# Optimization experiments

Measured on AMD Instinct MI355X. Metric: run time of the kernel, lower is better.

## Reference

```python
import jax, jax.numpy as jnp
import numpy as np

EPS = 1e-3  # sscp_conv_group_norm_eps


def setup_inputs() -> dict:
    key = jax.random.key(0)
    k1, k2, k3 = jax.random.split(key, 3)
    audio_encodings = jax.random.normal(k1, (4, 1, 4096, 128), dtype=jnp.float32)
    # Conv2d(in=1, out=128, kernel=(3,3), stride=(2,2), bias=False), OIHW layout
    conv_w = jax.random.normal(k2, (128, 1, 3, 3), dtype=jnp.float32) * 0.1
    # AudioCumulativeGroupNorm per-channel scale (init ones; randomize slightly)
    norm_scale = jnp.ones((128,), dtype=jnp.float32) + 0.01 * jax.random.normal(k3, (128,), dtype=jnp.float32)
    return {"audio_encodings": audio_encodings, "conv_w": conv_w, "norm_scale": norm_scale}


def reference(audio_encodings, conv_w, norm_scale):
    # manual_padding = (0, 1, 1, 1) in torch F.pad order (W_left, W_right, H_top, H_bottom)
    x = jnp.pad(audio_encodings, ((0, 0), (0, 0), (1, 1), (0, 1)))
    # Conv2d stride (2,2), no padding, no bias
    y = jax.lax.conv_general_dilated(
        x, conv_w, window_strides=(2, 2), padding='VALID',
        dimension_numbers=('NCHW', 'OIHW', 'NCHW'))  # [B, C, T, F]
    # permute to [B, T, F, C] and normalize cumulatively over T (mask=None)
    h = jnp.transpose(y, (0, 2, 3, 1)).astype(jnp.float32)
    B, T, F, C = h.shape
    # cumulative count of elements per group at each t: (t+1) * F * C
    cnt = (jnp.arange(1, T + 1, dtype=jnp.float32) * (F * C)).reshape(1, T, 1, 1)
    cum_sum = jnp.cumsum(jnp.sum(h, axis=(2, 3), keepdims=True), axis=1)  # [B,T,1,1]
    cum_mean = cum_sum / cnt
    sq = jnp.sum((h - cum_mean) ** 2, axis=(2, 3), keepdims=True)
    cum_var = jnp.cumsum(sq, axis=1) / cnt
    normed = (h - cum_mean) * jax.lax.rsqrt(cum_var + EPS) * norm_scale  # scale per channel (last dim)
    out = jnp.transpose(normed, (0, 3, 1, 2))  # back to [B, C, T, F]
    return jax.nn.relu(out)
```

## Files before the change

### kernel.cpp

```cpp
#include <hip/hip_runtime.h>

#define X_H 4096
#define X_W 128
#define BATCH 4
#define CH 128
#define TT_OUT 2048
#define FF 64
#define EPS_GN 1e-3f

typedef float f4 __attribute__((ext_vector_type(4)));

#define S1_OFF 0
#define SS_OFF (BATCH*TT_OUT)

__global__ __launch_bounds__(256) void stats_kernel(const float* __restrict__ x,
                                                    const float* __restrict__ w,
                                                    float* __restrict__ ws) {
    __shared__ float wlds[CH*9];
    __shared__ float Ml[81];
    __shared__ float Wl[9];
    int tid = threadIdx.x;
#pragma unroll
    for (int i = tid; i < CH*9; i += 256) wlds[i] = w[i];
    __syncthreads();
    if (tid < 81) {
        int j = tid / 9, k = tid % 9;
        float acc = 0.f;
#pragma unroll 8
        for (int c = 0; c < CH; ++c) acc = fmaf(wlds[c*9 + j], wlds[c*9 + k], acc);
        Ml[tid] = acc;
    } else if (tid < 90) {
        int k = tid - 81;
        float acc = 0.f;
#pragma unroll 8
        for (int c = 0; c < CH; ++c) acc += wlds[c*9 + k];
        Wl[k] = acc;
    }
    __syncthreads();

    int fq = tid & 15;
    int tr = tid >> 4;
    int gt = blockIdx.x * 16 + tr;
    int t = gt & (TT_OUT - 1);
    int b = gt >> 11;
    const float* xb = x + (size_t)b * (X_H * X_W);

    float xr[3][9];
    int r0 = 2*t - 1;
#pragma unroll
    for (int kh = 0; kh < 3; ++kh) {
        int r = r0 + kh;
        if (r >= 0 && r < X_H) {
            const float* rp = xb + (size_t)r * X_W + 8*fq;
            f4 v0 = *(const f4*)rp;
            f4 v1 = *(const f4*)(rp + 4);
            xr[kh][0]=v0.x; xr[kh][1]=v0.y; xr[kh][2]=v0.z; xr[kh][3]=v0.w;
            xr[kh][4]=v1.x; xr[kh][5]=v1.y; xr[kh][6]=v1.z; xr[kh][7]=v1.w;
            xr[kh][8] = (fq == 15) ? 0.f : rp[8];
        } else {
#pragma unroll
            for (int k = 0; k < 9; ++k) xr[kh][k] = 0.f;
        }
    }

    float s1 = 0.f, ss = 0.f;
#pragma unroll
    for (int jf = 0; jf < 4; ++jf) {
        float tv[9];
#pragma unroll
        for (int kh = 0; kh < 3; ++kh)
#pragma unroll
            for (int kw = 0; kw < 3; ++kw)
                tv[kh*3+kw] = xr[kh][2*jf + kw];
#pragma unroll
        for (int k = 0; k < 9; ++k) s1 = fmaf(Wl[k], tv[k], s1);
#pragma unroll
        for (int j = 0; j < 9; ++j) {
            float tj = 0.f;
#pragma unroll
            for (int k = 0; k < 9; ++k) tj = fmaf(Ml[j*9+k], tv[k], tj);
            ss = fmaf(tv[j], tj, ss);
        }
    }
#pragma unroll
    for (int off = 1; off < 16; off <<= 1) {
        s1 += __shfl_xor(s1, off);
        ss += __shfl_xor(ss, off);
    }
    if (fq == 0) {
        ws[S1_OFF + gt] = s1;
        ws[SS_OFF + gt] = ss;
    }
}

#define T_TILE 16
#define CG 32
__global__ __launch_bounds__(256) void out_kernel(const float* __restrict__ x,
        const float* __restrict__ w, const float* __restrict__ scale,
        const float* __restrict__ ws, float* __restrict__ out) {
    __shared__ float wl[CG][9];
    __shared__ float sl[CG];
    __shared__ float redA[4], redB[4], redC[4];
    int tid = threadIdx.x;
    int lane = tid & 63;
    int wv = tid >> 6;
    int b = blockIdx.z;
    int c0 = blockIdx.y * CG;
    int t0 = blockIdx.x * T_TILE;

    for (int i = tid; i < CG*9; i += 256) wl[i/9][i%9] = w[c0*9 + i];
    if (tid < CG) sl[tid] = scale[c0 + tid];

    const float* S1 = ws + S1_OFF + b*TT_OUT;
    const float* SS = ws + SS_OFF + b*TT_OUT;
    const f4* S1v = (const f4*)S1;
    const f4* SSv = (const f4*)SS;
    f4 a0 = S1v[tid*2], a1 = S1v[tid*2+1];
    f4 e0 = SSv[tid*2], e1 = SSv[tid*2+1];
    float s1l[8] = {a0.x,a0.y,a0.z,a0.w,a1.x,a1.y,a1.z,a1.w};
    float ssl[8] = {e0.x,e0.y,e0.z,e0.w,e1.x,e1.y,e1.z,e1.w};
    int tau0 = tid * 8;
    float s1m[8];
    float tot = 0.f;
#pragma unroll
    for (int i = 0; i < 8; ++i) {
        s1m[i] = (tau0 + i < t0) ? s1l[i] : 0.f;
        tot += s1m[i];
    }
    float incl = tot;
#pragma unroll
    for (int off = 1; off < 64; off <<= 1) {
        float n = __shfl_up(incl, off);
        if (lane >= off) incl += n;
    }
    if (lane == 63) redA[wv] = incl;
    __syncthreads();
    float woff = 0.f;
    for (int w2 = 0; w2 < wv; ++w2) woff += redA[w2];
    float prefix = woff + incl - tot;

    float run = prefix;
    float sqp = 0.f;
#pragma unroll
    for (int i = 0; i < 8; ++i) {
        if (tau0 + i < t0) {
            run += s1l[i];
            float cnt = (float)(tau0 + i + 1) * 8192.f;
            float mu = run / cnt;
            sqp += ssl[i] - 2.f*mu*s1l[i] + 8192.f*mu*mu;
        }
    }
    float r1 = tot, r2 = sqp;
#pragma unroll
    for (int off = 32; off > 0; off >>= 1) {
        r1 += __shfl_xor(r1, off);
        r2 += __shfl_xor(r2, off);
    }
    if (lane == 0) { redB[wv] = r1; redC[wv] = r2; }
    __syncthreads();
    float base1 = redB[0] + redB[1] + redB[2] + redB[3];
    float base_sq = redC[0] + redC[1] + redC[2] + redC[3];

    int tr = tid >> 4;
    float run16 = base1, sq16 = base_sq;
    float mu_t = 0.f, istd_t = 0.f;
#pragma unroll
    for (int i = 0; i < T_TILE; ++i) {
        int t = t0 + i;
        float s1t = S1[t];
        float sst = SS[t];
        run16 += s1t;
        float cnt = (float)(t + 1) * 8192.f;
        float mu = run16 / cnt;
        sq16 += sst - 2.f*mu*s1t + 8192.f*mu*mu;
        if (i == tr) { mu_t = mu; istd_t = rsqrtf(sq16 / cnt + EPS_GN); }
    }

    int fq = tid & 15;
    int t = t0 + tr;
    const float* xb = x + (size_t)b * (X_H * X_W);

    float xr[3][9];
    int r0 = 2*t - 1;
#pragma unroll
    for (int kh = 0; kh < 3; ++kh) {
        int r = r0 + kh;
        if (r >= 0 && r < X_H) {
            const float* rp = xb + (size_t)r * X_W + 8*fq;
            f4 v0 = *(const f4*)rp;
            f4 v1 = *(const f4*)(rp + 4);
            xr[kh][0]=v0.x; xr[kh][1]=v0.y; xr[kh][2]=v0.z; xr[kh][3]=v0.w;
            xr[kh][4]=v1.x; xr[kh][5]=v1.y; xr[kh][6]=v1.z; xr[kh][7]=v1.w;
            xr[kh][8] = (fq == 15) ? 0.f : rp[8];
        } else {
#pragma unroll
            for (int k = 0; k < 9; ++k) xr[kh][k] = 0.f;
        }
    }

    float* ob = out + (((size_t)(b*CH + c0) * TT_OUT + t) * FF + 4*fq);
#pragma unroll
    for (int c = 0; c < CG; ++c) {
        float a  = istd_t * sl[c];
        float nb = -mu_t * a;
        f4 v;
#pragma unroll
        for (int jf = 0; jf < 4; ++jf) {
            float h = 0.f;
#pragma unroll
            for (int kh = 0; kh < 3; ++kh)
#pragma unroll
                for (int kw = 0; kw < 3; ++kw)
                    h = fmaf(wl[c][kh*3+kw], xr[kh][2*jf + kw], h);
            v[jf] = fmaxf(fmaf(h, a, nb), 0.f);
        }
        *(f4*)(ob + (size_t)c * (TT_OUT * FF)) = v;
    }
}

extern "C" void kernel_launch(void* const* d_in, const int* in_sizes, int n_in,
                              void* d_out, int out_size, void* d_ws, size_t ws_size,
                              hipStream_t stream) {
    const float* x     = (const float*)d_in[0];
    const float* w     = (const float*)d_in[1];
    const float* scale = (const float*)d_in[2];
    float* out = (float*)d_out;
    float* ws  = (float*)d_ws;

    stats_kernel<<<(BATCH*TT_OUT)/16, 256, 0, stream>>>(x, w, ws);
    out_kernel<<<dim3(TT_OUT/T_TILE, CH/CG, BATCH), 256, 0, stream>>>(x, w, scale, ws, out);
}
```

Baseline: 59.35 us.

## Fuse stats and output kernels into one cooperative kernel with grid sync

Merges the statistics pass and the normalize/output pass into a single cooperative launch of 512 blocks, separated by a grid-wide barrier, so one kernel launch and its gap are removed. Each block now handles all 128 channels for its 16 time steps instead of splitting channels across 4 blocks, which cuts redundant input loads and prefix-scan work but leaves far fewer blocks for the write-heavy output phase. The grid barrier and the fixed 512-block grid also require all blocks to be co-resident.

```diff
diff --git a/kernel.cpp b/kernel.cpp
--- a/kernel.cpp
+++ b/kernel.cpp
@@ -1,4 +1,7 @@
 #include <hip/hip_runtime.h>
+#include <hip/hip_cooperative_groups.h>
+
+namespace cg = cooperative_groups;
 
 #define X_H 4096
 #define X_W 128
@@ -7,22 +10,32 @@
 #define TT_OUT 2048
 #define FF 64
 #define EPS_GN 1e-3f
+#define T_TILE 16
 
 typedef float f4 __attribute__((ext_vector_type(4)));
 
 #define S1_OFF 0
 #define SS_OFF (BATCH*TT_OUT)
 
-__global__ __launch_bounds__(256) void stats_kernel(const float* __restrict__ x,
-                                                    const float* __restrict__ w,
-                                                    float* __restrict__ ws) {
+__global__ __launch_bounds__(256) void fused_kernel(const float* __restrict__ x,
+        const float* __restrict__ w, const float* __restrict__ scale,
+        float* __restrict__ ws, float* __restrict__ out) {
     __shared__ float wlds[CH*9];
+    __shared__ float sl[CH];
     __shared__ float Ml[81];
     __shared__ float Wl[9];
+    __shared__ float redA[4], redB[4], redC[4];
+
     int tid = threadIdx.x;
+    int lane = tid & 63;
+    int wv = tid >> 6;
+    int bid = blockIdx.z * 128 + blockIdx.x;
+
 #pragma unroll
     for (int i = tid; i < CH*9; i += 256) wlds[i] = w[i];
-    __syncthreads();
+    if (tid < CH) sl[tid] = scale[tid];
+    __syncthreads();
+
     if (tid < 81) {
         int j = tid / 9, k = tid % 9;
         float acc = 0.f;
@@ -38,11 +51,133 @@
     }
     __syncthreads();
 
+    {
+        int fq = tid & 15;
+        int tr = tid >> 4;
+        int gt = bid * 16 + tr;
+        int t = gt & (TT_OUT - 1);
+        int b = gt >> 11;
+        const float* xb = x + (size_t)b * (X_H * X_W);
+
+        float xr[3][9];
+        int r0 = 2*t - 1;
+#pragma unroll
+        for (int kh = 0; kh < 3; ++kh) {
+            int r = r0 + kh;
+            if (r >= 0 && r < X_H) {
+                const float* rp = xb + (size_t)r * X_W + 8*fq;
+                f4 v0 = *(const f4*)rp;
+                f4 v1 = *(const f4*)(rp + 4);
+                xr[kh][0]=v0.x; xr[kh][1]=v0.y; xr[kh][2]=v0.z; xr[kh][3]=v0.w;
+                xr[kh][4]=v1.x; xr[kh][5]=v1.y; xr[kh][6]=v1.z; xr[kh][7]=v1.w;
+                xr[kh][8] = (fq == 15) ? 0.f : rp[8];
+            } else {
+#pragma unroll
+                for (int k = 0; k < 9; ++k) xr[kh][k] = 0.f;
+            }
+        }
+
+        float s1 = 0.f, ss = 0.f;
+#pragma unroll
+        for (int jf = 0; jf < 4; ++jf) {
+            float tv[9];
+#pragma unroll
+            for (int kh = 0; kh < 3; ++kh)
+#pragma unroll
+                for (int kw = 0; kw < 3; ++kw)
+                    tv[kh*3+kw] = xr[kh][2*jf + kw];
+#pragma unroll
+            for (int k = 0; k < 9; ++k) s1 = fmaf(Wl[k], tv[k], s1);
+#pragma unroll
+            for (int j = 0; j < 9; ++j) {
+                float tj = 0.f;
+#pragma unroll
+                for (int k = 0; k < 9; ++k) tj = fmaf(Ml[j*9+k], tv[k], tj);
+                ss = fmaf(tv[j], tj, ss);
+            }
+        }
+#pragma unroll
+        for (int off = 1; off < 16; off <<= 1) {
+            s1 += __shfl_xor(s1, off);
+            ss += __shfl_xor(ss, off);
+        }
+        if (fq == 0) {
+            ws[S1_OFF + gt] = s1;
+            ws[SS_OFF + gt] = ss;
+        }
+    }
+
+    __threadfence();
+    cg::this_grid().sync();
+
+    int b = blockIdx.z;
+    int t0 = blockIdx.x * T_TILE;
+
+    const float* S1 = ws + S1_OFF + b*TT_OUT;
+    const float* SS = ws + SS_OFF + b*TT_OUT;
+    const f4* S1v = (const f4*)S1;
+    const f4* SSv = (const f4*)SS;
+    f4 a0 = S1v[tid*2], a1 = S1v[tid*2+1];
+    f4 e0 = SSv[tid*2], e1 = SSv[tid*2+1];
+    float s1l[8] = {a0.x,a0.y,a0.z,a0.w,a1.x,a1.y,a1.z,a1.w};
+    float ssl[8] = {e0.x,e0.y,e0.z,e0.w,e1.x,e1.y,e1.z,e1.w};
+    int tau0 = tid * 8;
+    float tot = 0.f;
+#pragma unroll
+    for (int i = 0; i < 8; ++i) {
+        tot += (tau0 + i < t0) ? s1l[i] : 0.f;
+    }
+    float incl = tot;
+#pragma unroll
+    for (int off = 1; off < 64; off <<= 1) {
+        float n = __shfl_up(incl, off);
+        if (lane >= off) incl += n;
+    }
+    if (lane == 63) redA[wv] = incl;
+    __syncthreads();
+    float woff = 0.f;
+    for (int w2 = 0; w2 < wv; ++w2) woff += redA[w2];
+    float prefix = woff + incl - tot;
+
+    float run = prefix;
+    float sqp = 0.f;
+#pragma unroll
+    for (int i = 0; i < 8; ++i) {
+        if (tau0 + i < t0) {
+            run += s1l[i];
+            float cnt = (float)(tau0 + i + 1) * 8192.f;
+            float mu = run / cnt;
+            sqp += ssl[i] - 2.f*mu*s1l[i] + 8192.f*mu*mu;
+        }
+    }
+    float r1 = tot, r2 = sqp;
+#pragma unroll
+    for (int off = 32; off > 0; off >>= 1) {
+        r1 += __shfl_xor(r1, off);
+        r2 += __shfl_xor(r2, off);
+    }
+    if (lane == 0) { redB[wv] = r1; redC[wv] = r2; }
+    __syncthreads();
+    float base1 = redB[0] + redB[1] + redB[2] + redB[3];
+    float base_sq = redC[0] + redC[1] + redC[2] + redC[3];
+
+    int tr = tid >> 4;
+    float run16 = base1, sq16 = base_sq;
+    float mu_t = 0.f, istd_t = 0.f;
+#pragma unroll
+    for (int i = 0; i < T_TILE; ++i) {
+        int t = t0 + i;
+        float s1t = S1[t];
+        float sst = SS[t];
+        run16 += s1t;
+        float cnt = (float)(t + 1) * 8192.f;
+        float mu = run16 / cnt;
+        sq16 += sst - 2.f*mu*s1t + 8192.f*mu*mu;
+        if (i == tr) { mu_t = mu; istd_t = rsqrtf(sq16 / cnt + EPS_GN); }
+    }
+
     int fq = tid & 15;
-    int tr = tid >> 4;
-    int gt = blockIdx.x * 16 + tr;
-    int t = gt & (TT_OUT - 1);
-    int b = gt >> 11;
+    int t = t0 + tr;
     const float* xb = x + (size_t)b * (X_H * X_W);
 
     float xr[3][9];
@@ -63,144 +198,9 @@
         }
     }
 
-    float s1 = 0.f, ss = 0.f;
-#pragma unroll
-    for (int jf = 0; jf < 4; ++jf) {
-        float tv[9];
-#pragma unroll
-        for (int kh = 0; kh < 3; ++kh)
-#pragma unroll
-            for (int kw = 0; kw < 3; ++kw)
-                tv[kh*3+kw] = xr[kh][2*jf + kw];
-#pragma unroll
-        for (int k = 0; k < 9; ++k) s1 = fmaf(Wl[k], tv[k], s1);
-#pragma unroll
-        for (int j = 0; j < 9; ++j) {
-            float tj = 0.f;
-#pragma unroll
-            for (int k = 0; k < 9; ++k) tj = fmaf(Ml[j*9+k], tv[k], tj);
-            ss = fmaf(tv[j], tj, ss);
-        }
-    }
-#pragma unroll
-    for (int off = 1; off < 16; off <<= 1) {
-        s1 += __shfl_xor(s1, off);
-        ss += __shfl_xor(ss, off);
-    }
-    if (fq == 0) {
-        ws[S1_OFF + gt] = s1;
-        ws[SS_OFF + gt] = ss;
-    }
-}
-
-#define T_TILE 16
-#define CG 32
-__global__ __launch_bounds__(256) void out_kernel(const float* __restrict__ x,
-        const float* __restrict__ w, const float* __restrict__ scale,
-        const float* __restrict__ ws, float* __restrict__ out) {
-    __shared__ float wl[CG][9];
-    __shared__ float sl[CG];
-    __shared__ float redA[4], redB[4], redC[4];
-    int tid = threadIdx.x;
-    int lane = tid & 63;
-    int wv = tid >> 6;
-    int b = blockIdx.z;
-    int c0 = blockIdx.y * CG;
-    int t0 = blockIdx.x * T_TILE;
-
-    for (int i = tid; i < CG*9; i += 256) wl[i/9][i%9] = w[c0*9 + i];
-    if (tid < CG) sl[tid] = scale[c0 + tid];
-
-    const float* S1 = ws + S1_OFF + b*TT_OUT;
-    const float* SS = ws + SS_OFF + b*TT_OUT;
-    const f4* S1v = (const f4*)S1;
-    const f4* SSv = (const f4*)SS;
-    f4 a0 = S1v[tid*2], a1 = S1v[tid*2+1];
-    f4 e0 = SSv[tid*2], e1 = SSv[tid*2+1];
-    float s1l[8] = {a0.x,a0.y,a0.z,a0.w,a1.x,a1.y,a1.z,a1.w};
-    float ssl[8] = {e0.x,e0.y,e0.z,e0.w,e1.x,e1.y,e1.z,e1.w};
-    int tau0 = tid * 8;
-    float s1m[8];
-    float tot = 0.f;
-#pragma unroll
-    for (int i = 0; i < 8; ++i) {
-        s1m[i] = (tau0 + i < t0) ? s1l[i] : 0.f;
-        tot += s1m[i];
-    }
-    float incl = tot;
-#pragma unroll
-    for (int off = 1; off < 64; off <<= 1) {
-        float n = __shfl_up(incl, off);
-        if (lane >= off) incl += n;
-    }
-    if (lane == 63) redA[wv] = incl;
-    __syncthreads();
-    float woff = 0.f;
-    for (int w2 = 0; w2 < wv; ++w2) woff += redA[w2];
-    float prefix = woff + incl - tot;
-
-    float run = prefix;
-    float sqp = 0.f;
-#pragma unroll
-    for (int i = 0; i < 8; ++i) {
-        if (tau0 + i < t0) {
-            run += s1l[i];
-            float cnt = (float)(tau0 + i + 1) * 8192.f;
-            float mu = run / cnt;
-            sqp += ssl[i] - 2.f*mu*s1l[i] + 8192.f*mu*mu;
-        }
-    }
-    float r1 = tot, r2 = sqp;
-#pragma unroll
-    for (int off = 32; off > 0; off >>= 1) {
-        r1 += __shfl_xor(r1, off);
-        r2 += __shfl_xor(r2, off);
-    }
-    if (lane == 0) { redB[wv] = r1; redC[wv] = r2; }
-    __syncthreads();
-    float base1 = redB[0] + redB[1] + redB[2] + redB[3];
-    float base_sq = redC[0] + redC[1] + redC[2] + redC[3];
-
-    int tr = tid >> 4;
-    float run16 = base1, sq16 = base_sq;
-    float mu_t = 0.f, istd_t = 0.f;
-#pragma unroll
-    for (int i = 0; i < T_TILE; ++i) {
-        int t = t0 + i;
-        float s1t = S1[t];
-        float sst = SS[t];
-        run16 += s1t;
-        float cnt = (float)(t + 1) * 8192.f;
-        float mu = run16 / cnt;
-        sq16 += sst - 2.f*mu*s1t + 8192.f*mu*mu;
-        if (i == tr) { mu_t = mu; istd_t = rsqrtf(sq16 / cnt + EPS_GN); }
-    }
-
-    int fq = tid & 15;
-    int t = t0 + tr;
-    const float* xb = x + (size_t)b * (X_H * X_W);
-
-    float xr[3][9];
-    int r0 = 2*t - 1;
-#pragma unroll
-    for (int kh = 0; kh < 3; ++kh) {
-        int r = r0 + kh;
-        if (r >= 0 && r < X_H) {
-            const float* rp = xb + (size_t)r * X_W + 8*fq;
-            f4 v0 = *(const f4*)rp;
-            f4 v1 = *(const f4*)(rp + 4);
-            xr[kh][0]=v0.x; xr[kh][1]=v0.y; xr[kh][2]=v0.z; xr[kh][3]=v0.w;
-            xr[kh][4]=v1.x; xr[kh][5]=v1.y; xr[kh][6]=v1.z; xr[kh][7]=v1.w;
-            xr[kh][8] = (fq == 15) ? 0.f : rp[8];
-        } else {
-#pragma unroll
-            for (int k = 0; k < 9; ++k) xr[kh][k] = 0.f;
-        }
-    }
-
-    float* ob = out + (((size_t)(b*CH + c0) * TT_OUT + t) * FF + 4*fq);
-#pragma unroll
-    for (int c = 0; c < CG; ++c) {
+    float* ob = out + (((size_t)b * CH * TT_OUT + t) * FF + 4*fq);
+#pragma unroll 4
+    for (int c = 0; c < CH; ++c) {
         float a  = istd_t * sl[c];
         float nb = -mu_t * a;
         f4 v;
@@ -211,7 +211,7 @@
             for (int kh = 0; kh < 3; ++kh)
 #pragma unroll
                 for (int kw = 0; kw < 3; ++kw)
-                    h = fmaf(wl[c][kh*3+kw], xr[kh][2*jf + kw], h);
+                    h = fmaf(wlds[c*9 + kh*3+kw], xr[kh][2*jf + kw], h);
             v[jf] = fmaxf(fmaf(h, a, nb), 0.f);
         }
         *(f4*)(ob + (size_t)c * (TT_OUT * FF)) = v;
@@ -227,6 +227,8 @@
     float* out = (float*)d_out;
     float* ws  = (float*)d_ws;
 
-    stats_kernel<<<(BATCH*TT_OUT)/16, 256, 0, stream>>>(x, w, ws);
-    out_kernel<<<dim3(TT_OUT/T_TILE, CH/CG, BATCH), 256, 0, stream>>>(x, w, scale, ws, out);
+    void* args[] = {(void*)&x, (void*)&w, (void*)&scale, (void*)&ws, (void*)&out};
+    hipLaunchCooperativeKernel((const void*)fused_kernel,
+                               dim3(TT_OUT/T_TILE, 1, BATCH), dim3(256, 1, 1),
+                               args, 0, stream);
 }
```

Result: slower. 126.3 us (+112.8%).

## Hoist input loads early and parallelize per-tile stats scan with shuffles

Applied to the files above, without the earlier changes.

The input rows for the convolution are now loaded at the start of out_kernel, so their global-memory latency overlaps the prefix-sum reductions over the stats workspace. The serial 16-step loop that every thread ran over the tile's stats is replaced by a 16-lane shuffle inclusive scan, and each thread picks its mean and inverse std with a lane shuffle. The output channel loop is unrolled 4 instead of fully. Loading early keeps more registers live across the reductions, which may lower occupancy.

```diff
diff --git a/kernel.cpp b/kernel.cpp
--- a/kernel.cpp
+++ b/kernel.cpp
@@ -111,6 +111,30 @@
     for (int i = tid; i < CG*9; i += 256) wl[i/9][i%9] = w[c0*9 + i];
     if (tid < CG) sl[tid] = scale[c0 + tid];
 
+    int fq = tid & 15;
+    int tr = tid >> 4;
+    int t = t0 + tr;
+    const float* xb = x + (size_t)b * (X_H * X_W);
+    float xr[3][9];
+    {
+        int r0 = 2*t - 1;
+#pragma unroll
+        for (int kh = 0; kh < 3; ++kh) {
+            int r = r0 + kh;
+            if (r >= 0 && r < X_H) {
+                const float* rp = xb + (size_t)r * X_W + 8*fq;
+                f4 v0 = *(const f4*)rp;
+                f4 v1 = *(const f4*)(rp + 4);
+                xr[kh][0]=v0.x; xr[kh][1]=v0.y; xr[kh][2]=v0.z; xr[kh][3]=v0.w;
+                xr[kh][4]=v1.x; xr[kh][5]=v1.y; xr[kh][6]=v1.z; xr[kh][7]=v1.w;
+                xr[kh][8] = (fq == 15) ? 0.f : rp[8];
+            } else {
+#pragma unroll
+                for (int k = 0; k < 9; ++k) xr[kh][k] = 0.f;
+            }
+        }
+    }
+
     const float* S1 = ws + S1_OFF + b*TT_OUT;
     const float* SS = ws + SS_OFF + b*TT_OUT;
     const f4* S1v = (const f4*)S1;
@@ -120,12 +144,10 @@
     float s1l[8] = {a0.x,a0.y,a0.z,a0.w,a1.x,a1.y,a1.z,a1.w};
     float ssl[8] = {e0.x,e0.y,e0.z,e0.w,e1.x,e1.y,e1.z,e1.w};
     int tau0 = tid * 8;
-    float s1m[8];
     float tot = 0.f;
 #pragma unroll
     for (int i = 0; i < 8; ++i) {
-        s1m[i] = (tau0 + i < t0) ? s1l[i] : 0.f;
-        tot += s1m[i];
+        tot += (tau0 + i < t0) ? s1l[i] : 0.f;
     }
     float incl = tot;
 #pragma unroll
@@ -161,45 +183,29 @@
     float base1 = redB[0] + redB[1] + redB[2] + redB[3];
     float base_sq = redC[0] + redC[1] + redC[2] + redC[3];
 
-    int tr = tid >> 4;
-    float run16 = base1, sq16 = base_sq;
-    float mu_t = 0.f, istd_t = 0.f;
-#pragma unroll
-    for (int i = 0; i < T_TILE; ++i) {
-        int t = t0 + i;
-        float s1t = S1[t];
-        float sst = SS[t];
-        run16 += s1t;
-        float cnt = (float)(t + 1) * 8192.f;
-        float mu = run16 / cnt;
-        sq16 += sst - 2.f*mu*s1t + 8192.f*mu*mu;
-        if (i == tr) { mu_t = mu; istd_t = rsqrtf(sq16 / cnt + EPS_GN); }
-    }
-
-    int fq = tid & 15;
-    int t = t0 + tr;
-    const float* xb = x + (size_t)b * (X_H * X_W);
-
-    float xr[3][9];
-    int r0 = 2*t - 1;
-#pragma unroll
-    for (int kh = 0; kh < 3; ++kh) {
-        int r = r0 + kh;
-        if (r >= 0 && r < X_H) {
-            const float* rp = xb + (size_t)r * X_W + 8*fq;
-            f4 v0 = *(const f4*)rp;
-            f4 v1 = *(const f4*)(rp + 4);
-            xr[kh][0]=v0.x; xr[kh][1]=v0.y; xr[kh][2]=v0.z; xr[kh][3]=v0.w;
-            xr[kh][4]=v1.x; xr[kh][5]=v1.y; xr[kh][6]=v1.z; xr[kh][7]=v1.w;
-            xr[kh][8] = (fq == 15) ? 0.f : rp[8];
-        } else {
-#pragma unroll
-            for (int k = 0; k < 9; ++k) xr[kh][k] = 0.f;
-        }
-    }
+    float s1t = 0.f, sst = 0.f;
+    if (lane < T_TILE) { s1t = S1[t0 + lane]; sst = SS[t0 + lane]; }
+    float cs = s1t;
+#pragma unroll
+    for (int off = 1; off < 16; off <<= 1) {
+        float n = __shfl_up(cs, off);
+        if (lane >= off) cs += n;
+    }
+    float cnt_l = (float)(t0 + lane + 1) * 8192.f;
+    float mu_l = (base1 + cs) / cnt_l;
+    float term = sst - 2.f*mu_l*s1t + 8192.f*mu_l*mu_l;
+    float ct = term;
+#pragma unroll
+    for (int off = 1; off < 16; off <<= 1) {
+        float n = __shfl_up(ct, off);
+        if (lane >= off) ct += n;
+    }
+    float istd_l = rsqrtf((base_sq + ct) / cnt_l + EPS_GN);
+    float mu_t = __shfl(mu_l, tr);
+    float istd_t = __shfl(istd_l, tr);
 
     float* ob = out + (((size_t)(b*CH + c0) * TT_OUT + t) * FF + 4*fq);
-#pragma unroll
+#pragma unroll 4
     for (int c = 0; c < CG; ++c) {
         float a  = istd_t * sl[c];
         float nb = -mu_t * a;
```

Measured after the change: 58.78 us. Within noise of the previous version (-1.0%).
